# Kernel optimization log

Hardware: AMD Instinct MI355X
Metric: run time of the kernel (lower is better)

## Reference

```python
import jax, jax.numpy as jnp
import numpy as np

B, V, H, W = 2, 16, 512, 512
MAX_VARS, EMBED, P = 48, 1024, 8


def setup_inputs() -> dict:
    key = jax.random.key(0)
    k1, k2, k3, k4 = jax.random.split(key, 4)
    x = jax.random.normal(k1, (B, V, H, W), dtype=jnp.float32)
    vars_idx = jax.random.randint(k2, (V,), 0, MAX_VARS)
    # params scaled roughly like kaiming_uniform for fan_in = P*P
    bound = 1.0 / np.sqrt(P * P)
    proj_weights = jax.random.normal(k3, (MAX_VARS, EMBED, 1, P, P), dtype=jnp.float32) * bound
    proj_biases = jax.random.normal(k4, (MAX_VARS, EMBED), dtype=jnp.float32) * bound
    return {"x": x, "vars": vars_idx, "proj_weights": proj_weights, "proj_biases": proj_biases}


def reference(x, vars, proj_weights, proj_biases):
    # x: [B, V, H, W]; proj_weights: [max_vars, E, 1, p, p]; proj_biases: [max_vars, E]
    b, v, h_img, w_img = x.shape
    p = proj_weights.shape[-1]
    w_sel = proj_weights[vars][:, :, 0]          # [V, E, p, p]  (weight gather)
    b_sel = proj_biases[vars]                    # [V, E]
    hh, ww = h_img // p, w_img // p
    # non-overlapping patch extraction (stride == kernel) + per-variable matmul
    xp = x.reshape(b, v, hh, p, ww, p)           # [B, V, hh, p, ww, p]
    proj = jnp.einsum('bvhpwq,vepq->bvhwe', xp, w_sel)  # [B, V, hh, ww, E]
    # flatten=True: [B, V, L, E], L = hh*ww (matches reshape->flatten(3)->transpose(2,3))
    out = proj.reshape(b, v, hh * ww, -1) + b_sel[None, :, None, :]
    return out  # norm_layer=None -> Identity
```

## Files before the change

### kernel.cpp

```cpp
#include <hip/hip_runtime.h>
#include <hip/hip_bf16.h>

#define Bb 2
#define Vv 16
#define Hh 512
#define Ww 512
#define Kk 64
#define Ee 1024
#define Ll 4096

typedef __bf16 bf16x8 __attribute__((ext_vector_type(8)));
typedef __bf16 bf16x4 __attribute__((ext_vector_type(4)));
typedef float f32x4 __attribute__((ext_vector_type(4)));

#define LDSS 72

__global__ __launch_bounds__(256) void patch_embed_kernel(
    const float* __restrict__ x, const int* __restrict__ vars,
    const float* __restrict__ pw, const float* __restrict__ pb,
    float* __restrict__ out)
{
    __shared__ __bf16 Xs[128 * LDSS];
    __shared__ __bf16 Wt[128 * LDSS];

    const int tid = threadIdx.x;
    const int nt  = blockIdx.x;
    const int mt  = blockIdx.y;
    const int bv  = blockIdx.z;
    const int v   = bv & (Vv - 1);
    const int var = vars[v];

    const float4* xp = (const float4*)(x + ((size_t)bv * Hh + (size_t)mt * 16) * Ww);
    #pragma unroll
    for (int i = 0; i < 8; i++) {
        int f = tid + i * 256;
        float4 val = xp[f];
        int r  = f >> 7;
        int c4 = f & 127;
        int l  = ((r >> 3) << 6) + (c4 >> 1);
        int k  = ((r & 7) << 3) + ((c4 & 1) << 2);
        bf16x4 pk = { (__bf16)val.x, (__bf16)val.y, (__bf16)val.z, (__bf16)val.w };
        *(bf16x4*)&Xs[l * LDSS + k] = pk;
    }
    const float4* wp = (const float4*)(pw + ((size_t)var * Ee + (size_t)nt * 128) * Kk);
    #pragma unroll
    for (int i = 0; i < 8; i++) {
        int f = tid + i * 256;
        float4 val = wp[f];
        int row = f >> 4;
        int k   = (f & 15) << 2;
        bf16x4 pk = { (__bf16)val.x, (__bf16)val.y, (__bf16)val.z, (__bf16)val.w };
        *(bf16x4*)&Wt[row * LDSS + k] = pk;
    }

    const int lane = tid & 63;
    const int wv   = tid >> 6;
    const int wE   = (wv >> 1) << 6;
    const int wL   = (wv & 1) << 6;
    const int ln   = lane & 15;
    const int quad = lane >> 4;

    const float4* b4 = (const float4*)(pb + (size_t)var * Ee + nt * 128 + wE + quad * 4);
    f32x4 bias4[4];
    #pragma unroll
    for (int mi = 0; mi < 4; mi++) {
        float4 t = b4[mi * 4];
        f32x4 u = { t.x, t.y, t.z, t.w };
        bias4[mi] = u;
    }

    __syncthreads();

    f32x4 acc[4][4] = {};
    #pragma unroll
    for (int kh = 0; kh < 2; kh++) {
        bf16x8 wf[4], xf[4];
        #pragma unroll
        for (int mi = 0; mi < 4; mi++)
            wf[mi] = *(const bf16x8*)&Wt[(wE + mi * 16 + ln) * LDSS + kh * 32 + quad * 8];
        #pragma unroll
        for (int nj = 0; nj < 4; nj++)
            xf[nj] = *(const bf16x8*)&Xs[(wL + nj * 16 + ln) * LDSS + kh * 32 + quad * 8];
        #pragma unroll
        for (int mi = 0; mi < 4; mi++)
            #pragma unroll
            for (int nj = 0; nj < 4; nj++)
                acc[mi][nj] = __builtin_amdgcn_mfma_f32_16x16x32_bf16(
                    wf[mi], xf[nj], acc[mi][nj], 0, 0, 0);
    }

    float* outp = out + (size_t)bv * Ll * Ee;
    #pragma unroll
    for (int nj = 0; nj < 4; nj++) {
        size_t rowoff = (size_t)(mt * 128 + wL + nj * 16 + ln) * Ee
                      + (size_t)(nt * 128 + wE + quad * 4);
        #pragma unroll
        for (int mi = 0; mi < 4; mi++) {
            f32x4 val = acc[mi][nj] + bias4[mi];
            __builtin_nontemporal_store(val, (f32x4*)(outp + rowoff + mi * 16));
        }
    }
}

extern "C" void kernel_launch(void* const* d_in, const int* in_sizes, int n_in,
                              void* d_out, int out_size, void* d_ws, size_t ws_size,
                              hipStream_t stream) {
    const float* x    = (const float*)d_in[0];
    const int*   vars = (const int*)d_in[1];
    const float* pw   = (const float*)d_in[2];
    const float* pb   = (const float*)d_in[3];
    float* out = (float*)d_out;
    dim3 grid(Ee / 128, Ll / 128, Bb * Vv);
    dim3 block(256);
    hipLaunchKernelGGL(patch_embed_kernel, grid, block, 0, stream,
                       x, vars, pw, pb, out);
}
```

Measured before the change: 603.9 us.

## Loop over E tiles per block, keep X fragments in registers, drop LDS

Each block now covers all eight E tiles in a loop instead of launching one block per E tile. The X patch fragments are loaded once straight from global memory into registers, and weight fragments are read directly from global with a one-tile-ahead prefetch. Shared memory and the barrier are removed, and the bias is folded into the accumulator initialisation. This cuts redundant X reads and LDS traffic, but the grid becomes 8x smaller (1024 blocks) and the weight loads are uncoalesced per lane, which may hurt latency hiding on a store-bound kernel.

```diff
diff --git a/kernel.cpp b/kernel.cpp
--- a/kernel.cpp
+++ b/kernel.cpp
@@ -1,5 +1,4 @@
 #include <hip/hip_runtime.h>
-#include <hip/hip_bf16.h>
 
 #define Bb 2
 #define Vv 16
@@ -10,48 +9,24 @@
 #define Ll 4096
 
 typedef __bf16 bf16x8 __attribute__((ext_vector_type(8)));
-typedef __bf16 bf16x4 __attribute__((ext_vector_type(4)));
 typedef float f32x4 __attribute__((ext_vector_type(4)));
 
-#define LDSS 72
+static __device__ __forceinline__ bf16x8 cvt8(float4 a, float4 b) {
+    bf16x8 r = { (__bf16)a.x, (__bf16)a.y, (__bf16)a.z, (__bf16)a.w,
+                 (__bf16)b.x, (__bf16)b.y, (__bf16)b.z, (__bf16)b.w };
+    return r;
+}
 
 __global__ __launch_bounds__(256) void patch_embed_kernel(
     const float* __restrict__ x, const int* __restrict__ vars,
     const float* __restrict__ pw, const float* __restrict__ pb,
     float* __restrict__ out)
 {
-    __shared__ __bf16 Xs[128 * LDSS];
-    __shared__ __bf16 Wt[128 * LDSS];
-
     const int tid = threadIdx.x;
-    const int nt  = blockIdx.x;
-    const int mt  = blockIdx.y;
-    const int bv  = blockIdx.z;
+    const int mt  = blockIdx.x;
+    const int bv  = blockIdx.y;
     const int v   = bv & (Vv - 1);
     const int var = vars[v];
-
-    const float4* xp = (const float4*)(x + ((size_t)bv * Hh + (size_t)mt * 16) * Ww);
-    #pragma unroll
-    for (int i = 0; i < 8; i++) {
-        int f = tid + i * 256;
-        float4 val = xp[f];
-        int r  = f >> 7;
-        int c4 = f & 127;
-        int l  = ((r >> 3) << 6) + (c4 >> 1);
-        int k  = ((r & 7) << 3) + ((c4 & 1) << 2);
-        bf16x4 pk = { (__bf16)val.x, (__bf16)val.y, (__bf16)val.z, (__bf16)val.w };
-        *(bf16x4*)&Xs[l * LDSS + k] = pk;
-    }
-    const float4* wp = (const float4*)(pw + ((size_t)var * Ee + (size_t)nt * 128) * Kk);
-    #pragma unroll
-    for (int i = 0; i < 8; i++) {
-        int f = tid + i * 256;
-        float4 val = wp[f];
-        int row = f >> 4;
-        int k   = (f & 15) << 2;
-        bf16x4 pk = { (__bf16)val.x, (__bf16)val.y, (__bf16)val.z, (__bf16)val.w };
-        *(bf16x4*)&Wt[row * LDSS + k] = pk;
-    }
 
     const int lane = tid & 63;
     const int wv   = tid >> 6;
@@ -60,44 +35,79 @@
     const int ln   = lane & 15;
     const int quad = lane >> 4;
 
-    const float4* b4 = (const float4*)(pb + (size_t)var * Ee + nt * 128 + wE + quad * 4);
-    f32x4 bias4[4];
-    #pragma unroll
-    for (int mi = 0; mi < 4; mi++) {
-        float4 t = b4[mi * 4];
-        f32x4 u = { t.x, t.y, t.z, t.w };
-        bias4[mi] = u;
+    bf16x8 xf[2][4];
+    {
+        const float* xb = x + ((size_t)bv * Hh + (size_t)mt * 16 + (wL >> 3) + quad) * Ww;
+        #pragma unroll
+        for (int kh = 0; kh < 2; kh++) {
+            const float* xr = xb + (size_t)(kh * 4) * Ww;
+            #pragma unroll
+            for (int nj = 0; nj < 4; nj++) {
+                const float4* p = (const float4*)(xr + (nj * 16 + ln) * 8);
+                xf[kh][nj] = cvt8(p[0], p[1]);
+            }
+        }
     }
 
-    __syncthreads();
+    const float* wb = pw + ((size_t)var * Ee + wE + ln) * Kk + quad * 8;
+    const float* bb = pb + (size_t)var * Ee + wE + quad * 4;
+    float* ob = out + (size_t)bv * Ll * Ee
+                    + (size_t)(mt * 128 + wL + ln) * Ee + wE + quad * 4;
 
-    f32x4 acc[4][4] = {};
+    float4 wraw[2][4][2];
     #pragma unroll
-    for (int kh = 0; kh < 2; kh++) {
-        bf16x8 wf[4], xf[4];
-        #pragma unroll
-        for (int mi = 0; mi < 4; mi++)
-            wf[mi] = *(const bf16x8*)&Wt[(wE + mi * 16 + ln) * LDSS + kh * 32 + quad * 8];
-        #pragma unroll
-        for (int nj = 0; nj < 4; nj++)
-            xf[nj] = *(const bf16x8*)&Xs[(wL + nj * 16 + ln) * LDSS + kh * 32 + quad * 8];
-        #pragma unroll
-        for (int mi = 0; mi < 4; mi++)
-            #pragma unroll
-            for (int nj = 0; nj < 4; nj++)
-                acc[mi][nj] = __builtin_amdgcn_mfma_f32_16x16x32_bf16(
-                    wf[mi], xf[nj], acc[mi][nj], 0, 0, 0);
-    }
-
-    float* outp = out + (size_t)bv * Ll * Ee;
-    #pragma unroll
-    for (int nj = 0; nj < 4; nj++) {
-        size_t rowoff = (size_t)(mt * 128 + wL + nj * 16 + ln) * Ee
-                      + (size_t)(nt * 128 + wE + quad * 4);
+    for (int kh = 0; kh < 2; kh++)
         #pragma unroll
         for (int mi = 0; mi < 4; mi++) {
-            f32x4 val = acc[mi][nj] + bias4[mi];
-            __builtin_nontemporal_store(val, (f32x4*)(outp + rowoff + mi * 16));
+            const float4* p = (const float4*)(wb + (size_t)(mi * 16) * Kk + kh * 32);
+            wraw[kh][mi][0] = p[0];
+            wraw[kh][mi][1] = p[1];
+        }
+
+    #pragma unroll 1
+    for (int nt = 0; nt < 8; nt++) {
+        bf16x8 wf[2][4];
+        #pragma unroll
+        for (int kh = 0; kh < 2; kh++)
+            #pragma unroll
+            for (int mi = 0; mi < 4; mi++)
+                wf[kh][mi] = cvt8(wraw[kh][mi][0], wraw[kh][mi][1]);
+
+        f32x4 acc[4][4];
+        #pragma unroll
+        for (int mi = 0; mi < 4; mi++) {
+            float4 t = *(const float4*)(bb + nt * 128 + mi * 16);
+            f32x4 bias = { t.x, t.y, t.z, t.w };
+            #pragma unroll
+            for (int nj = 0; nj < 4; nj++) acc[mi][nj] = bias;
+        }
+
+        if (nt < 7) {
+            #pragma unroll
+            for (int kh = 0; kh < 2; kh++)
+                #pragma unroll
+                for (int mi = 0; mi < 4; mi++) {
+                    const float4* p = (const float4*)(wb + (size_t)((nt + 1) * 128 + mi * 16) * Kk + kh * 32);
+                    wraw[kh][mi][0] = p[0];
+                    wraw[kh][mi][1] = p[1];
+                }
+        }
+
+        #pragma unroll
+        for (int kh = 0; kh < 2; kh++)
+            #pragma unroll
+            for (int mi = 0; mi < 4; mi++)
+                #pragma unroll
+                for (int nj = 0; nj < 4; nj++)
+                    acc[mi][nj] = __builtin_amdgcn_mfma_f32_16x16x32_bf16(
+                        wf[kh][mi], xf[kh][nj], acc[mi][nj], 0, 0, 0);
+
+        #pragma unroll
+        for (int nj = 0; nj < 4; nj++) {
+            float* op = ob + (size_t)(nj * 16) * Ee + nt * 128;
+            #pragma unroll
+            for (int mi = 0; mi < 4; mi++)
+                __builtin_nontemporal_store(acc[mi][nj], (f32x4*)(op + mi * 16));
         }
     }
 }
@@ -110,7 +120,7 @@
     const float* pw   = (const float*)d_in[2];
     const float* pb   = (const float*)d_in[3];
     float* out = (float*)d_out;
-    dim3 grid(Ee / 128, Ll / 128, Bb * Vv);
+    dim3 grid(Ll / 128, Bb * Vv);
     dim3 block(256);
     hipLaunchKernelGGL(patch_embed_kernel, grid, block, 0, stream,
                        x, vars, pw, pb, out);
```

Result: slower. 639.0 us (+5.8%).
